# Optimization experiments

Hardware: AMD Instinct MI355X
Metric: run time of the kernel (lower is better)

The kernel has to match this reference:

```python
import jax, jax.numpy as jnp
import numpy as np

N = 100000   # num nodes
E = 3200000  # num edges (avg degree 32)
D = 256      # in_channels
H = 256      # hidden_dim
C = 1        # num_class
G = 512      # num graphs in batch


def setup_inputs() -> dict:
    key = jax.random.key(0)
    k = jax.random.split(key, 5)
    x = jax.random.normal(k[0], (N, D), dtype=jnp.float32)
    edge_index = jax.random.randint(k[1], (2, E), 0, N, dtype=jnp.int64)
    batch = jnp.sort(jax.random.randint(k[2], (N,), 0, G, dtype=jnp.int64))
    # GCNLayer.proj: Linear(D, H); model.lin: Linear(H, C)
    W1 = jax.random.normal(k[3], (H, D), dtype=jnp.float32) * 0.05
    b1 = jnp.zeros((H,), dtype=jnp.float32)
    W2 = jax.random.normal(k[4], (C, H), dtype=jnp.float32) * 0.05
    b2 = jnp.zeros((C,), dtype=jnp.float32)
    return {"x": x, "edge_index": edge_index, "batch": batch,
            "W1": W1, "b1": b1, "W2": W2, "b2": b2}


def reference(x, edge_index, batch, W1, b1, W2, b2):
    src, dst = edge_index[0], edge_index[1]
    # degree(edge_index[0]) over ORIGINAL edges (before self-loops), as in source
    deg = jnp.zeros((N,), x.dtype).at[src].add(jnp.asarray(1.0, x.dtype))
    norm = deg ** -0.5  # D^{-1/2}
    # (D^{-1/2} (A + I) D^{-1/2}) x
    # edge term: out[src] += norm[src] * norm[dst] * x[dst]
    msg = (norm[src] * norm[dst])[:, None] * x[dst]          # [E, D]
    agg = jax.ops.segment_sum(msg, src, num_segments=N)      # [N, D]
    agg = agg + (norm * norm)[:, None] * x                   # self-loop term
    h = jax.nn.relu(agg @ W1.T + b1)                          # [N, H]
    pooled = jax.ops.segment_max(h, batch, num_segments=G)   # [G, H]
    out = pooled @ W2.T + b2                                  # [G, 1]
    return jnp.squeeze(out, axis=1)                           # [G]
```

## Files before the change

### kernel.cpp

```cpp
#include <hip/hip_runtime.h>
#include <cstddef>

#define NN   100000
#define EE   3200000
#define GG   512
#define NBKT 1563
#define CAP  2432

typedef __attribute__((ext_vector_type(8))) short bf16x8;
typedef __attribute__((ext_vector_type(4))) float f32x4;
typedef __attribute__((ext_vector_type(8))) unsigned short u16x8;

static __device__ __forceinline__ unsigned short f2b(float f) {
  unsigned u = __float_as_uint(f);
  unsigned r = u + 0x7fffu + ((u >> 16) & 1u);
  return (unsigned short)(r >> 16);
}
static __device__ __forceinline__ float b2f(unsigned short s) {
  return __uint_as_float(((unsigned)s) << 16);
}

__global__ __launch_bounds__(1024) void k_bscatter(const int* __restrict__ src,
                                                   const int* __restrict__ dst,
                                                   int* __restrict__ gcur,
                                                   int* __restrict__ pk) {
  __shared__ int cnt[NBKT];
  __shared__ int base[NBKT];
  const int tid  = threadIdx.x;
  const int e_lo = blockIdx.x * (EE / 128);
  const int e_hi = e_lo + (EE / 128);

  for (int b = tid; b < NBKT; b += 1024) cnt[b] = 0;
  __syncthreads();
  for (int e = e_lo + tid; e < e_hi; e += 1024)
    atomicAdd(&cnt[src[e] >> 6], 1);
  __syncthreads();
  for (int b = tid; b < NBKT; b += 1024) {
    int c = cnt[b];
    base[b] = c ? atomicAdd(&gcur[b], c) : 0;
    cnt[b] = 0;
  }
  __syncthreads();
  for (int e = e_lo + tid; e < e_hi; e += 1024) {
    int s = src[e];
    int b = s >> 6;
    int idx = base[b] + atomicAdd(&cnt[b], 1);
    if (idx < CAP) pk[b * CAP + idx] = ((s & 63) << 17) | dst[e];
  }
}

__global__ __launch_bounds__(512) void k_prep(const int* __restrict__ gcur,
                                              const int* __restrict__ pk,
                                              const float* __restrict__ x,
                                              const float* __restrict__ w1,
                                              unsigned short* __restrict__ ybf,
                                              unsigned short* __restrict__ wbf,
                                              int* __restrict__ csr,
                                              int* __restrict__ ro) {
  __shared__ int hist[64], start[65], cur[64];
  const int tid = threadIdx.x;
  const int b   = blockIdx.x;
  const int n0  = b * 64;

  if (tid < 64) hist[tid] = 0;
  __syncthreads();
  const int szc = min(gcur[b], CAP);
  for (int j = tid; j < szc; j += 512)
    atomicAdd(&hist[pk[b * CAP + j] >> 17], 1);
  __syncthreads();
  if (tid < 64) {
    int s = 0;
    for (int t = 0; t < tid; ++t) s += hist[t];
    start[tid] = s; cur[tid] = s;
    if (tid == 63) start[64] = s + hist[63];
  }
  __syncthreads();
  for (int j = tid; j < szc; j += 512) {
    int w = pk[b * CAP + j];
    int pos = atomicAdd(&cur[w >> 17], 1);
    csr[b * CAP + pos] = w & 0x1FFFF;
  }
  if (tid < 65) ro[b * 65 + tid] = start[tid];

  for (int it = 0; it < 8; ++it) {
    int idx = it * 512 + tid;
    int row = idx >> 6, c4 = idx & 63;
    int n = n0 + row;
    if (n < NN) {
      float nr = rsqrtf((float)hist[row]);
      float4 v = ((const float4*)x)[(size_t)n * 64 + c4];
      ushort4 o;
      o.x = f2b(nr * v.x); o.y = f2b(nr * v.y); o.z = f2b(nr * v.z); o.w = f2b(nr * v.w);
      ((ushort4*)ybf)[(size_t)n * 64 + c4] = o;
    }
  }
  if (b < 64 && tid < 256) {
    int i = b * 256 + tid;
    float4 v = ((const float4*)w1)[i];
    ushort4 o;
    o.x = f2b(v.x); o.y = f2b(v.y); o.z = f2b(v.z); o.w = f2b(v.w);
    ((ushort4*)wbf)[i] = o;
  }
}

__global__ __launch_bounds__(512, 8) void k_fused4(const int* __restrict__ ro,
                                                   const int* __restrict__ csr,
                                                   const unsigned short* __restrict__ ybf,
                                                   const unsigned short* __restrict__ wbf,
                                                   const float* __restrict__ b1,
                                                   const int* __restrict__ batch,
                                                   int* __restrict__ pooled) {
  __shared__ __align__(16) unsigned short As[16][264];
  __shared__ int rs[17];
  __shared__ int bg[16];
  const int tid  = threadIdx.x;
  const int n0   = blockIdx.x * 16;
  const int bkt  = blockIdx.x >> 2;
  const int br   = (blockIdx.x & 3) * 16;
  const int wave = tid >> 6;
  const int lane = tid & 63;

  if (tid < 17) rs[tid] = ro[bkt * 65 + br + tid];
  else if (tid >= 64 && tid < 80) bg[tid - 64] = batch[n0 + tid - 64];
  __syncthreads();

  const int half = lane >> 5, l32 = lane & 31;
  const int il   = wave * 2 + half;
  const int i    = n0 + il;
  const u16x8* __restrict__ yr = (const u16x8*)ybf;
  const int* __restrict__ ce = csr + (size_t)bkt * CAP;

  u16x8 sv = yr[(size_t)i * 32 + l32];
  float acc[8];
#pragma unroll
  for (int c = 0; c < 8; ++c) acc[c] = b2f(sv[c]);

  int e = rs[il];
  const int e1 = rs[il + 1];
  const float ni = rsqrtf((float)(e1 - e));
  for (; e + 8 <= e1; e += 8) {
    int d0 = ce[e],     d1 = ce[e + 1], d2 = ce[e + 2], d3 = ce[e + 3];
    int d4 = ce[e + 4], d5 = ce[e + 5], d6 = ce[e + 6], d7 = ce[e + 7];
    u16x8 v0 = yr[(size_t)d0 * 32 + l32];
    u16x8 v1 = yr[(size_t)d1 * 32 + l32];
    u16x8 v2 = yr[(size_t)d2 * 32 + l32];
    u16x8 v3 = yr[(size_t)d3 * 32 + l32];
    u16x8 v4 = yr[(size_t)d4 * 32 + l32];
    u16x8 v5 = yr[(size_t)d5 * 32 + l32];
    u16x8 v6 = yr[(size_t)d6 * 32 + l32];
    u16x8 v7 = yr[(size_t)d7 * 32 + l32];
#pragma unroll
    for (int c = 0; c < 8; ++c)
      acc[c] += ((b2f(v0[c]) + b2f(v1[c])) + (b2f(v2[c]) + b2f(v3[c]))) +
                ((b2f(v4[c]) + b2f(v5[c])) + (b2f(v6[c]) + b2f(v7[c])));
  }
  for (; e + 4 <= e1; e += 4) {
    int d0 = ce[e], d1 = ce[e + 1], d2 = ce[e + 2], d3 = ce[e + 3];
    u16x8 v0 = yr[(size_t)d0 * 32 + l32];
    u16x8 v1 = yr[(size_t)d1 * 32 + l32];
    u16x8 v2 = yr[(size_t)d2 * 32 + l32];
    u16x8 v3 = yr[(size_t)d3 * 32 + l32];
#pragma unroll
    for (int c = 0; c < 8; ++c)
      acc[c] += (b2f(v0[c]) + b2f(v1[c])) + (b2f(v2[c]) + b2f(v3[c]));
  }
  for (; e < e1; ++e) {
    u16x8 v = yr[(size_t)ce[e] * 32 + l32];
#pragma unroll
    for (int c = 0; c < 8; ++c) acc[c] += b2f(v[c]);
  }
  u16x8 o;
#pragma unroll
  for (int c = 0; c < 8; ++c) o[c] = f2b(ni * acc[c]);
  *(u16x8*)&As[il][l32 * 8] = o;
  __syncthreads();

  const int r16 = lane & 15, quad = lane >> 4;
  f32x4 acc4[2];
#pragma unroll
  for (int t = 0; t < 2; ++t) acc4[t] = (f32x4){0.f, 0.f, 0.f, 0.f};
  for (int kc = 0; kc < 8; ++kc) {
    bf16x8 af = *(const bf16x8*)&As[r16][kc * 32 + quad * 8];
#pragma unroll
    for (int ct = 0; ct < 2; ++ct) {
      const int n = wave * 32 + ct * 16 + r16;
      bf16x8 bf = *(const bf16x8*)(wbf + (size_t)n * 256 + kc * 32 + quad * 8);
      acc4[ct] = __builtin_amdgcn_mfma_f32_16x16x32_bf16(af, bf, acc4[ct], 0, 0, 0);
    }
  }

  const int g0 = bg[0], g15 = bg[15];
  if (g0 == g15) {
#pragma unroll
    for (int ct = 0; ct < 2; ++ct) {
      const int col = wave * 32 + ct * 16 + r16;
      const float bias = b1[col];
      float m = 0.f;
#pragma unroll
      for (int r = 0; r < 4; ++r) m = fmaxf(m, acc4[ct][r] + bias);
      m = fmaxf(m, __shfl_xor(m, 16, 64));
      m = fmaxf(m, __shfl_xor(m, 32, 64));
      if (quad == 0) atomicMax(&pooled[g0 * 256 + col], __float_as_int(m));
    }
  } else {
#pragma unroll
    for (int ct = 0; ct < 2; ++ct) {
      const int col = wave * 32 + ct * 16 + r16;
      const float bias = b1[col];
      for (int g = g0; g <= g15; ++g) {
        float m = 0.f;
#pragma unroll
        for (int r = 0; r < 4; ++r) {
          const int row = quad * 4 + r;
          float v = fmaxf(acc4[ct][r] + bias, 0.f);
          if (bg[row] == g) m = fmaxf(m, v);
        }
        m = fmaxf(m, __shfl_xor(m, 16, 64));
        m = fmaxf(m, __shfl_xor(m, 32, 64));
        if (quad == 0) atomicMax(&pooled[g * 256 + col], __float_as_int(m));
      }
    }
  }
}

__global__ void k_out(const float* __restrict__ pooled, const float* __restrict__ w2,
                      const float* __restrict__ b2, float* __restrict__ out) {
  const int wave = threadIdx.x >> 6;
  const int lane = threadIdx.x & 63;
  const int g = blockIdx.x * 4 + wave;
  float4 p = ((const float4*)pooled)[g * 64 + lane];
  float4 w = ((const float4*)w2)[lane];
  float s = p.x * w.x + p.y * w.y + p.z * w.z + p.w * w.w;
  for (int off = 32; off; off >>= 1) s += __shfl_down(s, off, 64);
  if (lane == 0) out[g] = s + b2[0];
}

extern "C" void kernel_launch(void* const* d_in, const int* in_sizes, int n_in,
                              void* d_out, int out_size, void* d_ws, size_t ws_size,
                              hipStream_t stream) {
  const float* x     = (const float*)d_in[0];
  const int*   ei    = (const int*)d_in[1];
  const int*   batch = (const int*)d_in[2];
  const float* W1    = (const float*)d_in[3];
  const float* b1    = (const float*)d_in[4];
  const float* W2    = (const float*)d_in[5];
  const float* b2    = (const float*)d_in[6];
  const int* src = ei;
  const int* dst = ei + EE;
  float* out = (float*)d_out;

  size_t off = 0;
  auto carve = [&](size_t bytes) -> void* {
    void* p = (char*)d_ws + off;
    off += (bytes + 255) & ~(size_t)255;
    return p;
  };
  int*   pooled = (int*)carve((size_t)GG * 256 * 4);
  int*   gcur   = (int*)carve((size_t)NBKT * 4);
  unsigned short* ybf = (unsigned short*)carve((size_t)NN * 256 * 2);
  int*   pk     = (int*)carve((size_t)NBKT * CAP * 4);
  int*   csr    = (int*)carve((size_t)NBKT * CAP * 4);
  int*   ro     = (int*)carve((size_t)NBKT * 65 * 4);
  unsigned short* wbf = (unsigned short*)carve(256 * 256 * 2);

  hipMemsetAsync(pooled, 0, (size_t)GG * 256 * 4 + (size_t)NBKT * 4, stream);

  k_bscatter<<<128,  1024, 0, stream>>>(src, dst, gcur, pk);
  k_prep    <<<NBKT,  512, 0, stream>>>(gcur, pk, x, W1, ybf, wbf, csr, ro);
  k_fused4  <<<NN / 16, 512, 0, stream>>>(ro, csr, ybf, wbf, b1, batch, pooled);
  k_out     <<<GG / 4, 256, 0, stream>>>((const float*)pooled, W2, b2, out);
}
```

Baseline: 512.8 us.

## Replace single-pass bucket scatter with two-level radix partition of edges

```diff
diff --git a/kernel.cpp b/kernel.cpp
--- a/kernel.cpp
+++ b/kernel.cpp
@@ -1,11 +1,14 @@
 #include <hip/hip_runtime.h>
 #include <cstddef>
 
-#define NN   100000
-#define EE   3200000
-#define GG   512
-#define NBKT 1563
-#define CAP  2432
+#define NN    100000
+#define EE    3200000
+#define GG    512
+#define NBKT  1563
+#define CAP   2432
+#define CBINS 49
+#define CCAP  68000
+#define TT    4096
 
 typedef __attribute__((ext_vector_type(8))) short bf16x8;
 typedef __attribute__((ext_vector_type(4))) float f32x4;
@@ -20,32 +23,122 @@
   return __uint_as_float(((unsigned)s) << 16);
 }
 
-__global__ __launch_bounds__(1024) void k_bscatter(const int* __restrict__ src,
-                                                   const int* __restrict__ dst,
-                                                   int* __restrict__ gcur,
-                                                   int* __restrict__ pk) {
-  __shared__ int cnt[NBKT];
-  __shared__ int base[NBKT];
+__global__ __launch_bounds__(1024, 4) void k_split1(const int* __restrict__ src,
+                                                    const int* __restrict__ dst,
+                                                    int* __restrict__ ccur,
+                                                    int* __restrict__ cpk) {
+  __shared__ int hist[CBINS], st[CBINS], cur[CBINS], gbase[CBINS];
+  __shared__ int sorted[TT];
+  __shared__ unsigned char binof[TT];
   const int tid  = threadIdx.x;
-  const int e_lo = blockIdx.x * (EE / 128);
-  const int e_hi = e_lo + (EE / 128);
-
-  for (int b = tid; b < NBKT; b += 1024) cnt[b] = 0;
-  __syncthreads();
-  for (int e = e_lo + tid; e < e_hi; e += 1024)
-    atomicAdd(&cnt[src[e] >> 6], 1);
-  __syncthreads();
-  for (int b = tid; b < NBKT; b += 1024) {
-    int c = cnt[b];
-    base[b] = c ? atomicAdd(&gcur[b], c) : 0;
-    cnt[b] = 0;
-  }
-  __syncthreads();
-  for (int e = e_lo + tid; e < e_hi; e += 1024) {
-    int s = src[e];
-    int b = s >> 6;
-    int idx = base[b] + atomicAdd(&cnt[b], 1);
-    if (idx < CAP) pk[b * CAP + idx] = ((s & 63) << 17) | dst[e];
+  const int e_lo = blockIdx.x * (EE / 256);
+  const int e_hi = e_lo + (EE / 256);
+
+  for (int t0 = e_lo; t0 < e_hi; t0 += TT) {
+    const int tc = min(TT, e_hi - t0);
+    for (int k = tid; k < CBINS; k += 1024) hist[k] = 0;
+    __syncthreads();
+    int myk[4], myw[4];
+#pragma unroll
+    for (int r = 0; r < 4; ++r) {
+      int j = r * 1024 + tid;
+      myk[r] = -1;
+      if (j < tc) {
+        int s = src[t0 + j], d = dst[t0 + j];
+        myk[r] = s >> 11;
+        myw[r] = ((s & 2047) << 17) | d;
+        atomicAdd(&hist[myk[r]], 1);
+      }
+    }
+    __syncthreads();
+    if (tid < CBINS) {
+      int s = 0;
+      for (int t = 0; t < tid; ++t) s += hist[t];
+      st[tid] = s; cur[tid] = s;
+    }
+    __syncthreads();
+#pragma unroll
+    for (int r = 0; r < 4; ++r) {
+      if (myk[r] >= 0) {
+        int pos = atomicAdd(&cur[myk[r]], 1);
+        sorted[pos] = myw[r];
+        binof[pos] = (unsigned char)myk[r];
+      }
+    }
+    __syncthreads();
+    if (tid < CBINS) {
+      int c = cur[tid] - st[tid];
+      gbase[tid] = c ? atomicAdd(&ccur[tid], c) : 0;
+    }
+    __syncthreads();
+    for (int j = tid; j < tc; j += 1024) {
+      int k = binof[j];
+      int idx = gbase[k] + (j - st[k]);
+      if (idx < CCAP) cpk[(size_t)k * CCAP + idx] = sorted[j];
+    }
+    __syncthreads();
+  }
+}
+
+__global__ __launch_bounds__(1024, 4) void k_split2(const int* __restrict__ ccur,
+                                                    const int* __restrict__ cpk,
+                                                    int* __restrict__ gcur,
+                                                    int* __restrict__ pk) {
+  __shared__ int hist[32], st[32], cur[32], gbase[32];
+  __shared__ int sorted[TT];
+  __shared__ unsigned char binof[TT];
+  const int tid  = threadIdx.x;
+  const int c    = blockIdx.x >> 4;
+  const int sl   = blockIdx.x & 15;
+  const int clen = min(ccur[c], CCAP);
+  const int lo   = (int)((long long)clen * sl / 16);
+  const int hi   = (int)((long long)clen * (sl + 1) / 16);
+  const int* __restrict__ cp = cpk + (size_t)c * CCAP;
+
+  for (int t0 = lo; t0 < hi; t0 += TT) {
+    const int tc = min(TT, hi - t0);
+    if (tid < 32) hist[tid] = 0;
+    __syncthreads();
+    int myk[4], myw[4];
+#pragma unroll
+    for (int r = 0; r < 4; ++r) {
+      int j = r * 1024 + tid;
+      myk[r] = -1;
+      if (j < tc) {
+        int w    = cp[t0 + j];
+        int sl11 = w >> 17;
+        myk[r] = sl11 >> 6;
+        myw[r] = ((sl11 & 63) << 17) | (w & 0x1FFFF);
+        atomicAdd(&hist[myk[r]], 1);
+      }
+    }
+    __syncthreads();
+    if (tid < 32) {
+      int s = 0;
+      for (int t = 0; t < tid; ++t) s += hist[t];
+      st[tid] = s; cur[tid] = s;
+    }
+    __syncthreads();
+#pragma unroll
+    for (int r = 0; r < 4; ++r) {
+      if (myk[r] >= 0) {
+        int pos = atomicAdd(&cur[myk[r]], 1);
+        sorted[pos] = myw[r];
+        binof[pos] = (unsigned char)myk[r];
+      }
+    }
+    __syncthreads();
+    if (tid < 32) {
+      int cnum = cur[tid] - st[tid];
+      gbase[tid] = cnum ? atomicAdd(&gcur[c * 32 + tid], cnum) : 0;
+    }
+    __syncthreads();
+    for (int j = tid; j < tc; j += 1024) {
+      int k   = binof[j];
+      int idx = gbase[k] + (j - st[k]);
+      if (idx < CAP) pk[(size_t)(c * 32 + k) * CAP + idx] = sorted[j];
+    }
+    __syncthreads();
   }
 }
 
@@ -257,16 +350,20 @@
   };
   int*   pooled = (int*)carve((size_t)GG * 256 * 4);
   int*   gcur   = (int*)carve((size_t)NBKT * 4);
+  int*   ccur   = (int*)carve((size_t)CBINS * 4);
+  const size_t zlen = off;
   unsigned short* ybf = (unsigned short*)carve((size_t)NN * 256 * 2);
+  int*   cpk    = (int*)carve((size_t)CBINS * CCAP * 4);
   int*   pk     = (int*)carve((size_t)NBKT * CAP * 4);
   int*   csr    = (int*)carve((size_t)NBKT * CAP * 4);
   int*   ro     = (int*)carve((size_t)NBKT * 65 * 4);
   unsigned short* wbf = (unsigned short*)carve(256 * 256 * 2);
 
-  hipMemsetAsync(pooled, 0, (size_t)GG * 256 * 4 + (size_t)NBKT * 4, stream);
-
-  k_bscatter<<<128,  1024, 0, stream>>>(src, dst, gcur, pk);
-  k_prep    <<<NBKT,  512, 0, stream>>>(gcur, pk, x, W1, ybf, wbf, csr, ro);
-  k_fused4  <<<NN / 16, 512, 0, stream>>>(ro, csr, ybf, wbf, b1, batch, pooled);
-  k_out     <<<GG / 4, 256, 0, stream>>>((const float*)pooled, W2, b2, out);
-}
+  hipMemsetAsync(pooled, 0, zlen, stream);
+
+  k_split1<<<256,        1024, 0, stream>>>(src, dst, ccur, cpk);
+  k_split2<<<CBINS * 16, 1024, 0, stream>>>(ccur, cpk, gcur, pk);
+  k_prep  <<<NBKT,        512, 0, stream>>>(gcur, pk, x, W1, ybf, wbf, csr, ro);
+  k_fused4<<<NN / 16,     512, 0, stream>>>(ro, csr, ybf, wbf, b1, batch, pooled);
+  k_out   <<<GG / 4,      256, 0, stream>>>((const float*)pooled, W2, b2, out);
+}
```

Result: faster. 472.0 us (-8.0%).
